# Kernel tuning notes

Hardware: AMD Instinct MI355X
Metric: run time of the kernel (lower is better)

The kernel has to match this reference:

```python
import jax, jax.numpy as jnp
import numpy as np

V = 6890   # SMPL vertices
J = 24     # SMPL joints
NB = 10    # betas
P = 207    # pose blendshape basis = (J-1)*9
B = 1024
PARENTS = np.array([-1, 0, 0, 0, 1, 2, 3, 4, 5, 6, 7, 8, 9, 9, 9, 12, 13, 14, 16, 17, 18, 19, 20, 21])


def setup_inputs() -> dict:
    key = jax.random.key(0)
    ks = jax.random.split(key, 9)
    pose_axis_angle = jax.random.normal(ks[0], (B, 69), dtype=jnp.float32) * 0.2
    betas = jax.random.normal(ks[1], (B, NB), dtype=jnp.float32)
    global_orient = jax.random.normal(ks[2], (B, 3), dtype=jnp.float32) * 0.2
    v_template = jax.random.normal(ks[3], (V, 3), dtype=jnp.float32)
    shapedirs = jax.random.normal(ks[4], (V, 3, NB), dtype=jnp.float32) * 0.01
    posedirs = jax.random.normal(ks[5], (P, V * 3), dtype=jnp.float32) * 0.01
    jr = jax.random.uniform(ks[6], (J, V), dtype=jnp.float32)
    J_regressor = jr / jr.sum(-1, keepdims=True)
    jr17 = jax.random.uniform(ks[7], (17, V), dtype=jnp.float32)
    J_regressor_h36m = jr17 / jr17.sum(-1, keepdims=True)
    w = jax.random.uniform(ks[8], (V, J), dtype=jnp.float32)
    lbs_weights = w / w.sum(-1, keepdims=True)
    return {
        'pose_axis_angle': pose_axis_angle, 'betas': betas, 'global_orient': global_orient,
        'v_template': v_template, 'shapedirs': shapedirs, 'posedirs': posedirs,
        'J_regressor': J_regressor, 'J_regressor_h36m': J_regressor_h36m,
        'lbs_weights': lbs_weights,
    }


def rodrigues(rvec):
    # rvec: [N,3] axis-angle -> [N,3,3] rotation matrices
    angle = jnp.linalg.norm(rvec + 1e-8, axis=-1, keepdims=True)  # [N,1]
    axis = rvec / angle
    s = jnp.sin(angle)[..., None]
    c = jnp.cos(angle)[..., None]
    rx, ry, rz = axis[..., 0], axis[..., 1], axis[..., 2]
    z = jnp.zeros_like(rx)
    K = jnp.stack([z, -rz, ry, rz, z, -rx, -ry, rx, z], axis=-1).reshape(-1, 3, 3)
    I = jnp.eye(3, dtype=rvec.dtype)
    return I + s * K + (1.0 - c) * (K @ K)


def _lbs(pose_axis_angle, betas, global_orient, v_template, shapedirs, posedirs,
         J_regressor, J_regressor_h36m, lbs_weights):
    b = betas.shape[0]
    full_pose = jnp.concatenate([global_orient, pose_axis_angle], axis=1)  # [B,72]
    # shape blendshapes
    v_shaped = v_template + jnp.einsum('bl,vkl->bvk', betas, shapedirs)    # [B,V,3]
    Jrest = jnp.einsum('jv,bvk->bjk', J_regressor, v_shaped)               # [B,J,3]
    # pose to rotation matrices
    rot_mats = rodrigues(full_pose.reshape(-1, 3)).reshape(b, J, 3, 3)
    I3 = jnp.eye(3, dtype=rot_mats.dtype)
    pose_feature = (rot_mats[:, 1:] - I3).reshape(b, P)                    # [B,207]
    v_posed = v_shaped + (pose_feature @ posedirs).reshape(b, V, 3)
    # kinematic tree FK
    rel = Jrest.at[:, 1:].add(-Jrest[:, PARENTS[1:]])                      # relative joint offsets
    T = (jnp.zeros((b, J, 4, 4), dtype=rot_mats.dtype)
         .at[..., :3, :3].set(rot_mats)
         .at[..., :3, 3].set(rel)
         .at[..., 3, 3].set(1.0))
    chain = [T[:, 0]]
    for i in range(1, J):
        chain.append(chain[int(PARENTS[i])] @ T[:, i])
    G = jnp.stack(chain, axis=1)                                           # [B,J,4,4]
    posed_joints = G[:, :, :3, 3]
    # remove rest-pose joint locations to get skinning transforms
    A = G.at[:, :, :3, 3].add(-jnp.einsum('bjmn,bjn->bjm', G[:, :, :3, :3], Jrest))
    # linear blend skinning
    Tv = jnp.einsum('vj,bjmn->bvmn', lbs_weights, A)                       # [B,V,4,4]
    verts = jnp.einsum('bvmn,bvn->bvm', Tv[:, :, :3, :3], v_posed) + Tv[:, :, :3, 3]
    joints_from_verts = jnp.einsum('jv,bvk->bjk', J_regressor_h36m, verts)
    return verts, posed_joints, rot_mats, joints_from_verts


def reference(pose_axis_angle, betas, global_orient, v_template, shapedirs, posedirs,
              J_regressor, J_regressor_h36m, lbs_weights):
    verts, joints, rot_mats, jfv = _lbs(pose_axis_angle, betas, global_orient, v_template,
                                        shapedirs, posedirs, J_regressor, J_regressor_h36m,
                                        lbs_weights)
    # transl is None -> root-center (root is detached in torch)
    root = jax.lax.stop_gradient(joints[:, :1])
    root17 = jax.lax.stop_gradient(jfv[:, :1])
    return verts - root, joints - root, rot_mats, jfv - root17
```

## Files before the change

kernel.cpp:

```cpp
#include <hip/hip_runtime.h>
#include <hip/hip_bf16.h>

constexpr int kB  = 1024;
constexpr int kV  = 6890;
constexpr int kJ  = 24;
constexpr int kNB = 10;
constexpr int kP  = 207;
constexpr int kH  = 17;

constexpr int kN   = kV * 3;
constexpr int kKP  = 224;
constexpr int kNT  = 1296;
constexpr int kNP  = kNT * 16;
constexpr int kVC  = 862;
constexpr int kTB  = 8;

constexpr int kJsBlocks = kJ * 8;
constexpr int kPbBlocks = kNP / 64;
constexpr int kVB = (kV + 255) / 256;

constexpr size_t O_VERTS  = 0;
constexpr size_t O_JOINTS = (size_t)kB * kV * 3;
constexpr size_t O_ROT    = O_JOINTS + (size_t)kB * kJ * 3;
constexpr size_t O_JFV    = O_ROT + (size_t)kB * kJ * 9;

constexpr size_t WS_JSP  = 0;
constexpr size_t WS_A    = 8192;
constexpr size_t WS_ROOT = WS_A + (size_t)kB * 288;
constexpr size_t WS_ASWZ = WS_ROOT + 4096;
constexpr size_t WS_BSWZ = WS_ASWZ + 114688;

typedef __attribute__((ext_vector_type(8))) short short8;
typedef __attribute__((ext_vector_type(4))) float float4v;

__device__ __forceinline__ unsigned short f2bf(float f) {
    unsigned u = __float_as_uint(f);
    unsigned r = (u + 0x7FFFu + ((u >> 16) & 1u)) >> 16;
    return (unsigned short)r;
}

__device__ __forceinline__ bool amb0_is_weights(const float* __restrict__ amb0) {
    float s = 0.f;
    #pragma unroll
    for (int i = 0; i < kJ; i++) s += amb0[i];
    return fabsf(s - 1.0f) < 0.5f;
}

__device__ __forceinline__ size_t a_idx(int mtile, int minr, int k) {
    int kt = k >> 5, quad = (k >> 3) & 3, kin = k & 7;
    return ((size_t)(mtile * 7 + kt)) * 512 + (size_t)(quad * 128 + minr * 8 + kin);
}

__global__ __launch_bounds__(256) void k_sfb(
    const float* __restrict__ amb0,
    const float* __restrict__ amb1,
    const float* __restrict__ sd,
    const float* __restrict__ vt,
    const float* __restrict__ pd,
    float* __restrict__ partial,
    unsigned short* __restrict__ bswz)
{
    __shared__ unsigned short lds[kKP][68];
    __shared__ float red[4][33];

    int t = threadIdx.x;

    if (blockIdx.x < kJsBlocks) {
        const float* Jreg = amb0_is_weights(amb0) ? amb1 : amb0;
        int j = blockIdx.x >> 3;
        int c = blockIdx.x & 7;
        int lane = t & 63;
        int wave = t >> 6;

        float acc[33];
        #pragma unroll
        for (int i = 0; i < 33; i++) acc[i] = 0.f;

        int vend = min(kVC * (c + 1), kV);
        for (int v = kVC * c + t; v < vend; v += 256) {
            float w = Jreg[j * kV + v];
            const float* sdp = sd + (size_t)v * 30;
            #pragma unroll
            for (int k = 0; k < 3; k++) {
                #pragma unroll
                for (int l = 0; l < kNB; l++)
                    acc[k * 11 + l] += w * sdp[k * 10 + l];
                acc[k * 11 + 10] += w * vt[v * 3 + k];
            }
        }
        #pragma unroll
        for (int off = 32; off > 0; off >>= 1) {
            #pragma unroll
            for (int i = 0; i < 33; i++)
                acc[i] += __shfl_down(acc[i], off, 64);
        }
        if (lane == 0) {
            #pragma unroll
            for (int i = 0; i < 33; i++) red[wave][i] = acc[i];
        }
        __syncthreads();
        if (t < 33) {
            float s = red[0][t] + red[1][t] + red[2][t] + red[3][t];
            partial[((size_t)j * 8 + c) * 33 + t] = s;
        }
    } else {
        int g = blockIdx.x - kJsBlocks;
        int n0 = g * 64;

        for (int kbase = 0; kbase < kKP; kbase += 4) {
            int k = kbase + (t >> 6);
            int nl = t & 63;
            int n = n0 + nl;
            float val = 0.f;
            if (n < kN) {
                if (k < kP)                 val = pd[(size_t)k * kN + n];
                else if (k < kP + kNB)      val = sd[(size_t)n * kNB + (k - kP)];
                else if (k == kP + kNB)     val = vt[n];
            }
            lds[k][nl] = f2bf(val);
        }
        __syncthreads();

        #pragma unroll 1
        for (int tt = 0; tt < 4; tt++) {
            int ntile = g * 4 + tt;
            #pragma unroll 1
            for (int kt = 0; kt < 7; kt++) {
                size_t base = ((size_t)ntile * 7 + kt) * 512;
                #pragma unroll
                for (int u = 0; u < 2; u++) {
                    int e = t * 2 + u;
                    int quad = e >> 7, rem = e & 127;
                    int nin = rem >> 3, kin = rem & 7;
                    int k = kt * 32 + quad * 8 + kin;
                    bswz[base + e] = lds[k][tt * 16 + nin];
                }
            }
        }
    }
}

__global__ __launch_bounds__(64) void k_pose(
    const float* __restrict__ pose,
    const float* __restrict__ betas,
    const float* __restrict__ gor,
    const float* __restrict__ jsp,
    float* __restrict__ wsA,
    float* __restrict__ wsRoot,
    unsigned short* __restrict__ aswz,
    float* __restrict__ out)
{
    __shared__ float Rsh[kJ][9];
    __shared__ float Jr[kJ][3];
    __shared__ float G[kJ][12];

    int b = blockIdx.x;
    int t = threadIdx.x;
    int mtile = b >> 4, minr = b & 15;

    if (t < kJ) {
        float rx, ry, rz;
        if (t == 0) {
            rx = gor[b * 3 + 0]; ry = gor[b * 3 + 1]; rz = gor[b * 3 + 2];
        } else {
            int o = b * 69 + (t - 1) * 3;
            rx = pose[o]; ry = pose[o + 1]; rz = pose[o + 2];
        }
        float ex = rx + 1e-8f, ey = ry + 1e-8f, ez = rz + 1e-8f;
        float ang = sqrtf(ex * ex + ey * ey + ez * ez);
        float x = rx / ang, y = ry / ang, z = rz / ang;
        float s = sinf(ang), c = cosf(ang), oc = 1.0f - c;
        float r[9];
        r[0] = 1.0f - oc * (y * y + z * z);
        r[1] = -s * z + oc * (x * y);
        r[2] =  s * y + oc * (x * z);
        r[3] =  s * z + oc * (x * y);
        r[4] = 1.0f - oc * (x * x + z * z);
        r[5] = -s * x + oc * (y * z);
        r[6] = -s * y + oc * (x * z);
        r[7] =  s * x + oc * (y * z);
        r[8] = 1.0f - oc * (x * x + y * y);
        #pragma unroll
        for (int i = 0; i < 9; i++) Rsh[t][i] = r[i];
        float* ro = out + O_ROT + (size_t)b * (kJ * 9) + (size_t)t * 9;
        #pragma unroll
        for (int i = 0; i < 9; i++) ro[i] = r[i];
        if (t >= 1) {
            #pragma unroll
            for (int i = 0; i < 9; i++) {
                int k = (t - 1) * 9 + i;
                float val = r[i] - ((i == 0 || i == 4 || i == 8) ? 1.0f : 0.0f);
                aswz[a_idx(mtile, minr, k)] = f2bf(val);
            }
        }
        float bt[kNB];
        #pragma unroll
        for (int l = 0; l < kNB; l++) bt[l] = betas[b * kNB + l];
        #pragma unroll
        for (int k2 = 0; k2 < 3; k2++) {
            float row[11];
            #pragma unroll
            for (int i = 0; i < 11; i++) row[i] = 0.f;
            #pragma unroll
            for (int c8 = 0; c8 < 8; c8++) {
                const float* pp = jsp + ((size_t)t * 8 + c8) * 33 + k2 * 11;
                #pragma unroll
                for (int i = 0; i < 11; i++) row[i] += pp[i];
            }
            float acc = row[10];
            #pragma unroll
            for (int l = 0; l < kNB; l++) acc += bt[l] * row[l];
            Jr[t][k2] = acc;
        }
    } else if (t < 41 + kJ) {
        int idx = t - kJ;
        if (idx < 17) {
            int k = kP + idx;
            float val = 0.f;
            if (idx < kNB)          val = betas[b * kNB + idx];
            else if (k == kP + kNB) val = 1.0f;
            aswz[a_idx(mtile, minr, k)] = f2bf(val);
        }
    }
    __syncthreads();

    if (t == 0) {
        const int par[kJ] = {-1,0,0,0,1,2,3,4,5,6,7,8,9,9,9,12,13,14,16,17,18,19,20,21};
        #pragma unroll
        for (int m = 0; m < 3; m++) {
            #pragma unroll
            for (int n = 0; n < 3; n++) G[0][m * 4 + n] = Rsh[0][m * 3 + n];
            G[0][m * 4 + 3] = Jr[0][m];
        }
        for (int i = 1; i < kJ; i++) {
            int p = par[i];
            float rel[3];
            #pragma unroll
            for (int k = 0; k < 3; k++) rel[k] = Jr[i][k] - Jr[p][k];
            #pragma unroll
            for (int m = 0; m < 3; m++) {
                float g0 = G[p][m * 4 + 0], g1 = G[p][m * 4 + 1], g2 = G[p][m * 4 + 2];
                #pragma unroll
                for (int n = 0; n < 3; n++) {
                    G[i][m * 4 + n] = g0 * Rsh[i][0 * 3 + n]
                                    + g1 * Rsh[i][1 * 3 + n]
                                    + g2 * Rsh[i][2 * 3 + n];
                }
                G[i][m * 4 + 3] = g0 * rel[0] + g1 * rel[1] + g2 * rel[2]
                                + G[p][m * 4 + 3];
            }
        }
    }
    __syncthreads();

    if (t < kJ) {
        float* Aj = wsA + (size_t)b * 288 + (size_t)t * 12;
        float* jo = out + O_JOINTS + (size_t)b * (kJ * 3) + (size_t)t * 3;
        #pragma unroll
        for (int m = 0; m < 3; m++) {
            float g0 = G[t][m * 4 + 0], g1 = G[t][m * 4 + 1], g2 = G[t][m * 4 + 2];
            Aj[m * 4 + 0] = g0;
            Aj[m * 4 + 1] = g1;
            Aj[m * 4 + 2] = g2;
            Aj[m * 4 + 3] = G[t][m * 4 + 3]
                          - (g0 * Jr[t][0] + g1 * Jr[t][1] + g2 * Jr[t][2]);
            jo[m] = G[t][m * 4 + 3] - G[0][m * 4 + 3];
        }
        if (t == 0) {
            #pragma unroll
            for (int k = 0; k < 3; k++) wsRoot[b * 3 + k] = G[0][k * 4 + 3];
        }
    }
}

__global__ __launch_bounds__(256) void k_gemm(
    const unsigned short* __restrict__ A,
    const unsigned short* __restrict__ B,
    float* __restrict__ out)
{
    int tid = threadIdx.x;
    int lane = tid & 63;
    int wid = tid >> 6;
    int m0t = blockIdx.y * 8 + (wid >> 1) * 4;
    int n0t = blockIdx.x * 8 + (wid & 1) * 4;

    float4v acc[4][4];
    #pragma unroll
    for (int i = 0; i < 4; i++)
        #pragma unroll
        for (int j = 0; j < 4; j++)
            acc[i][j] = (float4v){0.f, 0.f, 0.f, 0.f};

    #pragma unroll
    for (int kt = 0; kt < 7; kt++) {
        short8 a[4], b[4];
        #pragma unroll
        for (int i = 0; i < 4; i++)
            a[i] = *(const short8*)(A + ((size_t)(m0t + i) * 7 + kt) * 512 + lane * 8);
        #pragma unroll
        for (int j = 0; j < 4; j++)
            b[j] = *(const short8*)(B + ((size_t)(n0t + j) * 7 + kt) * 512 + lane * 8);
        #pragma unroll
        for (int i = 0; i < 4; i++)
            #pragma unroll
            for (int j = 0; j < 4; j++)
                acc[i][j] = __builtin_amdgcn_mfma_f32_16x16x32_bf16(
                    a[i], b[j], acc[i][j], 0, 0, 0);
    }

    int rbase = (lane >> 4) * 4;
    int col = lane & 15;
    #pragma unroll
    for (int i = 0; i < 4; i++) {
        #pragma unroll
        for (int j = 0; j < 4; j++) {
            int n = (n0t + j) * 16 + col;
            if (n < kN) {
                #pragma unroll
                for (int reg = 0; reg < 4; reg++) {
                    int brow = (m0t + i) * 16 + rbase + reg;
                    out[O_VERTS + (size_t)brow * kN + n] = acc[i][j][reg];
                }
            }
        }
    }
}

__global__ __launch_bounds__(256, 4) void k_lbs(
    const float* __restrict__ amb0,
    const float* __restrict__ amb1,
    const float* __restrict__ wsA,
    const float* __restrict__ wsRoot,
    float* __restrict__ out)
{
    const float* W = amb0_is_weights(amb0) ? amb0 : amb1;

    int t = threadIdx.x;
    int v = blockIdx.x * 256 + t;
    int b0 = blockIdx.y * kTB;
    bool active = (v < kV);
    int vc = active ? v : (kV - 1);

    float w[kJ];
    {
        const float4v* Wv4 = (const float4v*)(W + (size_t)vc * kJ);
        #pragma unroll
        for (int q = 0; q < 6; q++) {
            float4v x = Wv4[q];
            w[q * 4 + 0] = x[0]; w[q * 4 + 1] = x[1];
            w[q * 4 + 2] = x[2]; w[q * 4 + 3] = x[3];
        }
    }

    #pragma unroll 1
    for (int tb = 0; tb < kTB; tb++) {
        int b = b0 + tb;
        const float4v* A4 = (const float4v*)(wsA + (size_t)b * 288);
        float T0[4] = {0.f, 0.f, 0.f, 0.f};
        float T1[4] = {0.f, 0.f, 0.f, 0.f};
        float T2[4] = {0.f, 0.f, 0.f, 0.f};
        #pragma unroll
        for (int j = 0; j < kJ; j++) {
            float wj = w[j];
            float4v a0 = A4[j * 3 + 0];
            float4v a1 = A4[j * 3 + 1];
            float4v a2 = A4[j * 3 + 2];
            #pragma unroll
            for (int q = 0; q < 4; q++) {
                T0[q] += wj * a0[q];
                T1[q] += wj * a1[q];
                T2[q] += wj * a2[q];
            }
        }
        float r0 = wsRoot[(size_t)b * 3 + 0];
        float r1 = wsRoot[(size_t)b * 3 + 1];
        float r2 = wsRoot[(size_t)b * 3 + 2];
        if (active) {
            float* op = out + O_VERTS + ((size_t)b * kV + v) * 3;
            float x = op[0], y = op[1], z = op[2];
            op[0] = T0[0] * x + T0[1] * y + T0[2] * z + T0[3] - r0;
            op[1] = T1[0] * x + T1[1] * y + T1[2] * z + T1[3] - r1;
            op[2] = T2[0] * x + T2[1] * y + T2[2] * z + T2[3] - r2;
        }
    }
}

__global__ __launch_bounds__(256) void k_jfv(
    const float* __restrict__ Jh,
    const float* __restrict__ verts,
    float* __restrict__ out)
{
    int b = blockIdx.x;
    int t = threadIdx.x;
    int lane = t & 63, wave = t >> 6;

    float acc[kH * 3];
    #pragma unroll
    for (int i = 0; i < kH * 3; i++) acc[i] = 0.f;

    for (int v = t; v < kV; v += 256) {
        const float* vp = verts + ((size_t)b * kV + v) * 3;
        float vx = vp[0], vy = vp[1], vz = vp[2];
        #pragma unroll
        for (int j = 0; j < kH; j++) {
            float wj = Jh[(size_t)j * kV + v];
            acc[j * 3 + 0] += wj * vx;
            acc[j * 3 + 1] += wj * vy;
            acc[j * 3 + 2] += wj * vz;
        }
    }
    #pragma unroll
    for (int off = 32; off > 0; off >>= 1) {
        #pragma unroll
        for (int i = 0; i < kH * 3; i++)
            acc[i] += __shfl_down(acc[i], off, 64);
    }
    __shared__ float red[4][kH * 3];
    __shared__ float fin[kH * 3];
    if (lane == 0) {
        #pragma unroll
        for (int i = 0; i < kH * 3; i++) red[wave][i] = acc[i];
    }
    __syncthreads();
    if (t < kH * 3)
        fin[t] = red[0][t] + red[1][t] + red[2][t] + red[3][t];
    __syncthreads();
    if (t < kH * 3) {
        out[O_JFV + (size_t)b * 51 + t] = fin[t] - fin[t % 3];
    }
}

extern "C" void kernel_launch(void* const* d_in, const int* in_sizes, int n_in,
                              void* d_out, int out_size, void* d_ws, size_t ws_size,
                              hipStream_t stream) {
    const float *pose = nullptr, *betas = nullptr, *gor = nullptr, *vt = nullptr,
                *sd = nullptr, *pd = nullptr, *Jh = nullptr;
    const float *amb0 = nullptr, *amb1 = nullptr;
    for (int i = 0; i < n_in; i++) {
        const float* p = (const float*)d_in[i];
        switch (in_sizes[i]) {
            case 70656:   pose  = p; break;
            case 10240:   betas = p; break;
            case 3072:    gor   = p; break;
            case 20670:   vt    = p; break;
            case 206700:  sd    = p; break;
            case 4278690: pd    = p; break;
            case 117130:  Jh    = p; break;
            case 165360:  if (!amb0) amb0 = p; else amb1 = p; break;
            default: break;
        }
    }

    float* ws = (float*)d_ws;
    float* jsp     = ws + WS_JSP;
    float* wsA     = ws + WS_A;
    float* wsRoot  = ws + WS_ROOT;
    unsigned short* aswz = (unsigned short*)(ws + WS_ASWZ);
    unsigned short* bswz = (unsigned short*)(ws + WS_BSWZ);

    float* out = (float*)d_out;

    k_sfb  <<<dim3(kJsBlocks + kPbBlocks), dim3(256), 0, stream>>>(
        amb0, amb1, sd, vt, pd, jsp, bswz);
    k_pose <<<dim3(kB),                 dim3(64),  0, stream>>>(
        pose, betas, gor, jsp, wsA, wsRoot, aswz, out);
    k_gemm <<<dim3(kNT / 8, kB / 128),  dim3(256), 0, stream>>>(aswz, bswz, out);
    k_lbs  <<<dim3(kVB, kB / kTB),      dim3(256), 0, stream>>>(
        amb0, amb1, wsA, wsRoot, out);
    k_jfv  <<<dim3(kB),                 dim3(256), 0, stream>>>(
        Jh, out + O_VERTS, out);
}
```

Baseline: 287.8 us.

## Restructure h36m joint regression to split joints across waves and batch four samples

The joint-from-vertices kernel now assigns one h36m joint per wave (wave 0 also takes joint 16) and processes four batch samples per 1024-thread block. Each regressor weight row is read once and reused across four samples. Register pressure drops from 51 accumulators to 24, and the cross-wave shared-memory reduction goes away. Separately, the LBS kernel's batch tile shrinks from 8 to 4 to launch more blocks. The trade-off is that every wave rereads the same vertex data, which shifts load onto the caches.

```diff
diff --git a/kernel.cpp b/kernel.cpp
--- a/kernel.cpp
+++ b/kernel.cpp
@@ -13,11 +13,12 @@
 constexpr int kNT  = 1296;
 constexpr int kNP  = kNT * 16;
 constexpr int kVC  = 862;
-constexpr int kTB  = 8;
+constexpr int kTB  = 4;
 
 constexpr int kJsBlocks = kJ * 8;
 constexpr int kPbBlocks = kNP / 64;
 constexpr int kVB = (kV + 255) / 256;
+constexpr int kJB  = 4;
 
 constexpr size_t O_VERTS  = 0;
 constexpr size_t O_JOINTS = (size_t)kB * kV * 3;
@@ -385,48 +386,61 @@
     }
 }
 
-__global__ __launch_bounds__(256) void k_jfv(
+__global__ __launch_bounds__(1024) void k_jfv(
     const float* __restrict__ Jh,
     const float* __restrict__ verts,
     float* __restrict__ out)
 {
-    int b = blockIdx.x;
+    int b0 = blockIdx.x * kJB;
     int t = threadIdx.x;
-    int lane = t & 63, wave = t >> 6;
-
-    float acc[kH * 3];
-    #pragma unroll
-    for (int i = 0; i < kH * 3; i++) acc[i] = 0.f;
-
-    for (int v = t; v < kV; v += 256) {
-        const float* vp = verts + ((size_t)b * kV + v) * 3;
-        float vx = vp[0], vy = vp[1], vz = vp[2];
-        #pragma unroll
-        for (int j = 0; j < kH; j++) {
-            float wj = Jh[(size_t)j * kV + v];
-            acc[j * 3 + 0] += wj * vx;
-            acc[j * 3 + 1] += wj * vy;
-            acc[j * 3 + 2] += wj * vz;
+    int wave = t >> 6, lane = t & 63;
+    int j0 = wave;
+    bool has2 = (wave == 0);
+
+    float acc0[kJB][3], acc1[kJB][3];
+    #pragma unroll
+    for (int bb = 0; bb < kJB; bb++)
+        #pragma unroll
+        for (int k = 0; k < 3; k++) { acc0[bb][k] = 0.f; acc1[bb][k] = 0.f; }
+
+    const float* Jr0 = Jh + (size_t)j0 * kV;
+    const float* Jr1 = Jh + (size_t)16 * kV;
+
+    for (int v = lane; v < kV; v += 64) {
+        float w0 = Jr0[v];
+        float w1 = has2 ? Jr1[v] : 0.f;
+        #pragma unroll
+        for (int bb = 0; bb < kJB; bb++) {
+            const float* vp = verts + ((size_t)(b0 + bb) * kV + v) * 3;
+            float vx = vp[0], vy = vp[1], vz = vp[2];
+            acc0[bb][0] += w0 * vx; acc0[bb][1] += w0 * vy; acc0[bb][2] += w0 * vz;
+            acc1[bb][0] += w1 * vx; acc1[bb][1] += w1 * vy; acc1[bb][2] += w1 * vz;
         }
     }
     #pragma unroll
     for (int off = 32; off > 0; off >>= 1) {
         #pragma unroll
-        for (int i = 0; i < kH * 3; i++)
-            acc[i] += __shfl_down(acc[i], off, 64);
-    }
-    __shared__ float red[4][kH * 3];
-    __shared__ float fin[kH * 3];
+        for (int bb = 0; bb < kJB; bb++)
+            #pragma unroll
+            for (int k = 0; k < 3; k++) {
+                acc0[bb][k] += __shfl_down(acc0[bb][k], off, 64);
+                acc1[bb][k] += __shfl_down(acc1[bb][k], off, 64);
+            }
+    }
+    __shared__ float fin[kJB][52];
     if (lane == 0) {
         #pragma unroll
-        for (int i = 0; i < kH * 3; i++) red[wave][i] = acc[i];
+        for (int bb = 0; bb < kJB; bb++)
+            #pragma unroll
+            for (int k = 0; k < 3; k++) {
+                fin[bb][j0 * 3 + k] = acc0[bb][k];
+                if (has2) fin[bb][48 + k] = acc1[bb][k];
+            }
     }
     __syncthreads();
-    if (t < kH * 3)
-        fin[t] = red[0][t] + red[1][t] + red[2][t] + red[3][t];
-    __syncthreads();
-    if (t < kH * 3) {
-        out[O_JFV + (size_t)b * 51 + t] = fin[t] - fin[t % 3];
+    if (t < kJB * 51) {
+        int bb = t / 51, i = t - bb * 51;
+        out[O_JFV + (size_t)(b0 + bb) * 51 + i] = fin[bb][i] - fin[bb][i % 3];
     }
 }
 
@@ -467,6 +481,6 @@
     k_gemm <<<dim3(kNT / 8, kB / 128),  dim3(256), 0, stream>>>(aswz, bswz, out);
     k_lbs  <<<dim3(kVB, kB / kTB),      dim3(256), 0, stream>>>(
         amb0, amb1, wsA, wsRoot, out);
-    k_jfv  <<<dim3(kB),                 dim3(256), 0, stream>>>(
+    k_jfv  <<<dim3(kB / kJB),           dim3(1024), 0, stream>>>(
         Jh, out + O_VERTS, out);
 }
```

Measured after the change: 312.6 us. 8.6% more time.
